# Kernel tuning notes

Hardware: AMD Instinct MI355X
Metric: run time of the kernel (lower is better)

## Reference

```python
import jax, jax.numpy as jnp
import numpy as np

B, Z, L = 256, 256, 8
C0, H0, W0 = 128, 8, 8
O = C0 * H0 * W0  # 8192


def _conv_transpose(x, w, b):
    """Torch ConvTranspose2d(k=4, s=2, p=1) equivalent.
    w: torch layout (in_ch, out_ch, kH, kW).
    Implemented as lhs-dilated conv with flipped, transposed kernel; pad = k-1-p = 2.
    """
    wt = jnp.flip(w, (2, 3)).transpose(1, 0, 2, 3)  # (out, in, kh, kw)
    y = jax.lax.conv_general_dilated(
        x, wt, window_strides=(1, 1), padding=[(2, 2), (2, 2)],
        lhs_dilation=(2, 2), dimension_numbers=('NCHW', 'OIHW', 'NCHW'))
    return y + b[None, :, None, None]


def setup_inputs() -> dict:
    key = jax.random.key(0)
    ks = jax.random.split(key, 6)
    return {
        'x': jax.random.normal(ks[0], (B, Z), jnp.float32),
        'gw': jax.random.normal(ks[1], (Z, L), jnp.float32) * (2.0 / (Z + L)) ** 0.5,  # xavier_normal
        'gb': jnp.zeros((L,), jnp.float32),
        'pw': jax.random.normal(ks[2], (O, Z, L), jnp.float32) * (1.0 / Z) ** 0.5,  # kaiming linear
        'pb': jnp.zeros((O, L), jnp.float32),
        'w1': jax.random.normal(ks[3], (C0, 64, 4, 4), jnp.float32) * 0.02,
        'b1': jnp.zeros((64,), jnp.float32),
        'w2': jax.random.normal(ks[4], (64, 32, 4, 4), jnp.float32) * 0.02,
        'b2': jnp.zeros((32,), jnp.float32),
        'w3': jax.random.normal(ks[5], (32, 3, 4, 4), jnp.float32) * 0.02,
        'b3': jnp.zeros((3,), jnp.float32),
    }


def reference(x, gw, gb, pw, pb, w1, b1, w2, b2, w3, b3):
    # --- ME mixture of linear experts (linear projection) ---
    g = jax.nn.softmax(x @ gw + gb, axis=1)               # (B, L)
    # Per-expert linear outputs, then gate-weighted sum. Mathematically equal to
    # torch's (pw @ gatings) per-sample weight followed by bmm with x, but avoids
    # the (B, O, Z) intermediate.
    expert_out = jnp.einsum('bi,oil->bol', x, pw)          # (B, O, L)
    out = jnp.einsum('bol,bl->bo', expert_out, g) + g @ pb.T  # (B, O)
    # --- conv-transpose decoder stack ---
    h = out.reshape(B, C0, H0, W0)
    h = jax.nn.relu(_conv_transpose(h, w1, b1))            # (B, 64, 16, 16)
    h = jax.nn.relu(_conv_transpose(h, w2, b2))            # (B, 32, 32, 32)
    h = _conv_transpose(h, w3, b3)                         # (B, 3, 64, 64)
    return h
```

## Files before the change

kernel.cpp:

```cpp
#include <hip/hip_runtime.h>

typedef __bf16 bf16;
typedef __bf16 bf16x8 __attribute__((ext_vector_type(8)));
typedef float f32x4 __attribute__((ext_vector_type(4)));

__device__ __forceinline__ f32x4 mfma16(bf16x8 a, bf16x8 b, f32x4 c) {
  return __builtin_amdgcn_mfma_f32_16x16x32_bf16(a, b, c, 0, 0, 0);
}

__device__ __forceinline__ void gload16(const void* g, void* l) {
  __builtin_amdgcn_global_load_lds(
      (const __attribute__((address_space(1))) void*)g,
      (__attribute__((address_space(3))) void*)(uint32_t)(size_t)l, 16, 0, 0);
}

__global__ __launch_bounds__(256) void gating_kernel(
    const float* __restrict__ x, const float* __restrict__ gw,
    const float* __restrict__ gb, bf16* __restrict__ xgb,
    float* __restrict__ gbuf) {
  const int b = blockIdx.x, tid = threadIdx.x;
  __shared__ float xs[256];
  __shared__ float gs[8];
  xs[tid] = x[b * 256 + tid];
  __syncthreads();
  if (tid < 8) {
    float acc = gb[tid];
    for (int i = 0; i < 256; ++i) acc += xs[i] * gw[i * 8 + tid];
    gs[tid] = acc;
  }
  __syncthreads();
  if (tid == 0) {
    float m = gs[0];
    for (int l = 1; l < 8; ++l) m = fmaxf(m, gs[l]);
    float s = 0.f, e[8];
    for (int l = 0; l < 8; ++l) { e[l] = expf(gs[l] - m); s += e[l]; }
    float inv = 1.f / s;
    for (int l = 0; l < 8; ++l) gs[l] = e[l] * inv;
  }
  __syncthreads();
  if (tid < 8) gbuf[b * 8 + tid] = gs[tid];
  bf16* dst = xgb + (size_t)b * 2048;
  for (int k = tid; k < 2048; k += 256)
    dst[k] = (bf16)(xs[k >> 3] * gs[k & 7]);
}

__global__ __launch_bounds__(256) void convert_pw_kernel(
    const float* __restrict__ pw, bf16* __restrict__ pwb) {
  const size_t base = (size_t)blockIdx.x * 2048 + threadIdx.x * 8;
  float4 v0 = *(const float4*)(pw + base);
  float4 v1 = *(const float4*)(pw + base + 4);
  bf16x8 r;
  r[0] = (bf16)v0.x; r[1] = (bf16)v0.y; r[2] = (bf16)v0.z; r[3] = (bf16)v0.w;
  r[4] = (bf16)v1.x; r[5] = (bf16)v1.y; r[6] = (bf16)v1.z; r[7] = (bf16)v1.w;
  *(bf16x8*)(pwb + base) = r;
}

template <int CIN, int COUT, int COUTP>
__global__ __launch_bounds__(256) void convert_w_kernel(
    const float* __restrict__ w, bf16* __restrict__ wp) {
  constexpr int K = 4 * CIN;
  constexpr int total = 4 * COUTP * K;
  int idx = blockIdx.x * 256 + threadIdx.x;
  if (idx >= total) return;
  int ic = idx & (CIN - 1);
  int t = (idx / CIN) & 3;
  int oc = (idx / K) % COUTP;
  int p = idx / (K * COUTP);
  bf16 v = (bf16)0.f;
  if (oc < COUT) {
    int py = p >> 1, px = p & 1, tyi = t >> 1, txi = t & 1;
    int ky = py == 0 ? (tyi ? 3 : 1) : (tyi ? 2 : 0);
    int kx = px == 0 ? (txi ? 3 : 1) : (txi ? 2 : 0);
    v = (bf16)w[((ic * COUT + oc) * 4 + ky) * 4 + kx];
  }
  wp[idx] = v;
}

template <int HP, int WP, int C>
__global__ __launch_bounds__(256) void border_zero_kernel(bf16* __restrict__ buf) {
  constexpr int NCELL = 2 * WP + 2 * (HP - 2);
  constexpr int C8 = C / 8;
  int idx = blockIdx.x * 256 + threadIdx.x;
  if (idx >= 256 * NCELL * C8) return;
  int c8 = idx % C8;
  int rem = idx / C8;
  int cell = rem % NCELL;
  int b = rem / NCELL;
  int y, x;
  if (cell < WP) { y = 0; x = cell; }
  else if (cell < 2 * WP) { y = HP - 1; x = cell - WP; }
  else { int r2 = cell - 2 * WP; y = 1 + (r2 >> 1); x = (r2 & 1) ? WP - 1 : 0; }
  bf16x8 z = {};
  *(bf16x8*)(buf + ((size_t)(b * HP + y) * WP + x) * C + c8 * 8) = z;
}

__global__ __launch_bounds__(256) void me_gemm_kernel(
    const bf16* __restrict__ pwb, const bf16* __restrict__ xgb,
    const float* __restrict__ pb, const float* __restrict__ gbuf,
    bf16* __restrict__ h0t) {
  __shared__ char sAB[32768];
  const int tid = threadIdx.x, wv = tid >> 6, l = tid & 63;
  const int lr = l & 15, lkg = l >> 4;
  const int wm = wv >> 1, wn = wv & 1;
  const int oM0 = blockIdx.x * 64, bN0 = blockIdx.y * 64;

  const int r1 = tid >> 3, cc1 = tid & 7;
  const int sb1 = (cc1 * 16) ^ ((r1 & 7) << 4);
  const int r2 = r1 + 32;
  const int sb2 = (cc1 * 16) ^ ((r2 & 7) << 4);
  const bf16* pA1 = pwb + (size_t)(oM0 + r1) * 2048 + (sb1 >> 1);
  const bf16* pA2 = pwb + (size_t)(oM0 + r2) * 2048 + (sb2 >> 1);
  const bf16* pB1 = xgb + (size_t)(bN0 + r1) * 2048 + (sb1 >> 1);
  const bf16* pB2 = xgb + (size_t)(bN0 + r2) * 2048 + (sb2 >> 1);
  char* lb0 = sAB + wv * 1024;

  gload16(pA1, lb0);
  gload16(pA2, lb0 + 4096);
  gload16(pB1, lb0 + 8192);
  gload16(pB2, lb0 + 12288);

  int raddrA[2][2], raddrB[2][2];
#pragma unroll
  for (int m = 0; m < 2; ++m) {
    int ra = wm * 32 + m * 16 + lr;
#pragma unroll
    for (int ks = 0; ks < 2; ++ks)
      raddrA[m][ks] = ra * 128 + ((ks * 64 + lkg * 16) ^ ((ra & 7) << 4));
  }
#pragma unroll
  for (int n = 0; n < 2; ++n) {
    int rb = wn * 32 + n * 16 + lr;
#pragma unroll
    for (int ks = 0; ks < 2; ++ks)
      raddrB[n][ks] = 8192 + rb * 128 + ((ks * 64 + lkg * 16) ^ ((rb & 7) << 4));
  }

  f32x4 acc[2][2] = {};
  __syncthreads();
#pragma unroll 2
  for (int kt = 0; kt < 32; ++kt) {
    const int cur = (kt & 1) * 16384;
    if (kt < 31) {
      char* lb = sAB + (((kt + 1) & 1) * 16384) + wv * 1024;
      const int ke = (kt + 1) * 64;
      gload16(pA1 + ke, lb);
      gload16(pA2 + ke, lb + 4096);
      gload16(pB1 + ke, lb + 8192);
      gload16(pB2 + ke, lb + 12288);
    }
    bf16x8 af[2][2], bfr[2][2];
#pragma unroll
    for (int ks = 0; ks < 2; ++ks) {
#pragma unroll
      for (int m = 0; m < 2; ++m)
        af[m][ks] = *(const bf16x8*)(sAB + cur + raddrA[m][ks]);
#pragma unroll
      for (int n = 0; n < 2; ++n)
        bfr[n][ks] = *(const bf16x8*)(sAB + cur + raddrB[n][ks]);
    }
#pragma unroll
    for (int ks = 0; ks < 2; ++ks)
#pragma unroll
      for (int m = 0; m < 2; ++m)
#pragma unroll
        for (int n = 0; n < 2; ++n)
          acc[m][n] = mfma16(af[m][ks], bfr[n][ks], acc[m][n]);
    __syncthreads();
  }

  float4 g0[2], g1[2];
#pragma unroll
  for (int n = 0; n < 2; ++n) {
    int b = bN0 + wn * 32 + n * 16 + lr;
    g0[n] = *(const float4*)(gbuf + b * 8);
    g1[n] = *(const float4*)(gbuf + b * 8 + 4);
  }
#pragma unroll
  for (int m = 0; m < 2; ++m)
#pragma unroll
    for (int r = 0; r < 4; ++r) {
      int o = oM0 + wm * 32 + m * 16 + lkg * 4 + r;
      float4 p0 = *(const float4*)(pb + o * 8);
      float4 p1 = *(const float4*)(pb + o * 8 + 4);
      int c = o >> 6, y = (o >> 3) & 7, xx = o & 7;
#pragma unroll
      for (int n = 0; n < 2; ++n) {
        int b = bN0 + wn * 32 + n * 16 + lr;
        float bias = g0[n].x * p0.x + g0[n].y * p0.y + g0[n].z * p0.z + g0[n].w * p0.w +
                     g1[n].x * p1.x + g1[n].y * p1.y + g1[n].z * p1.z + g1[n].w * p1.w;
        h0t[((size_t)(b * 10 + y + 1) * 10 + xx + 1) * 128 + c] = (bf16)(acc[m][n][r] + bias);
      }
    }
}

template <int CIN, int H, int YB, int COUTP, int WM, int NF, int SWM,
          bool WLDS, int INIT, int WIT, bool RELU, bool F32OUT, int SIN_SZ, int SW_SZ>
__global__ __launch_bounds__(256) void convt_kernel(
    const bf16* __restrict__ in, const bf16* __restrict__ wp,
    const float* __restrict__ bias, bf16* __restrict__ out,
    float* __restrict__ fout) {
  constexpr int W = H, WROW = W + 2, ROWB = CIN * 2, GRS = ROWB / 16;
  constexpr int LGR = (GRS == 16) ? 4 : (GRS == 8) ? 3 : 2;
  constexpr int LW = (W == 8) ? 3 : (W == 16) ? 4 : 5;
  constexpr int K = 4 * CIN;
  constexpr int CHUNKS = (YB + 2) * WROW * GRS;
  constexpr int WGR = K / 8;
  __shared__ char sIn[SIN_SZ];
  __shared__ char sW[SW_SZ];

  const int tid = threadIdx.x, wv = tid >> 6, l = tid & 63;
  const int nyb = H / YB;
  const int img = blockIdx.x / nyb, y0 = (blockIdx.x % nyb) * YB;
  const int p = blockIdx.y, py = p >> 1, px = p & 1;

#pragma unroll
  for (int it = 0; it < INIT; ++it) {
    int t = it * 256 + tid;
    int tc = t < CHUNKS ? t : CHUNKS - 1;
    int pix = tc >> LGR, cc = tc & (GRS - 1);
    int ly = pix / WROW, lx = pix % WROW;
    int sb = (cc * 16) ^ ((pix & SWM) << 4);
    gload16(in + ((size_t)((img * (H + 2) + y0 + ly) * (W + 2) + lx)) * CIN + (sb >> 1),
            sIn + it * 4096 + wv * 1024);
  }
  if constexpr (WLDS) {
#pragma unroll
    for (int it = 0; it < WIT; ++it) {
      int t = it * 256 + tid;
      int oc = t / WGR, cc = t % WGR;
      int sb = (cc * 16) ^ ((oc & 7) << 4);
      gload16(wp + (size_t)(p * COUTP + oc) * K + (sb >> 1), sW + it * 4096 + wv * 1024);
    }
  }
  __syncthreads();

  const int lr = l & 15, lkg = l >> 4;
  const int wm = wv & (WM - 1), wn = wv / WM;
  int pcen[2];
#pragma unroll
  for (int m = 0; m < 2; ++m) {
    int r = wm * 32 + m * 16 + lr;
    pcen[m] = ((r >> LW) + 1) * WROW + (r & (W - 1)) + 1;
  }

  f32x4 acc[2][NF] = {};
#pragma unroll 4
  for (int kk = 0; kk < K; kk += 32) {
    const int t4 = kk / CIN;
    const int tyi = t4 >> 1, txi = t4 & 1;
    const int dy = (py == 0) ? (tyi ? -1 : 0) : (tyi ? 0 : 1);
    const int dx = (px == 0) ? (txi ? -1 : 0) : (txi ? 0 : 1);
    const int icb = (kk % CIN) * 2 + lkg * 16;
    bf16x8 av[2], bv[NF];
#pragma unroll
    for (int m = 0; m < 2; ++m) {
      int pixd = pcen[m] + dy * WROW + dx;
      av[m] = *(const bf16x8*)(sIn + pixd * ROWB + (icb ^ ((pixd & SWM) << 4)));
    }
#pragma unroll
    for (int n = 0; n < NF; ++n) {
      int oc = (wn * NF + n) * 16 + lr;
      if constexpr (WLDS) {
        int kb = kk * 2 + lkg * 16;
        bv[n] = *(const bf16x8*)(sW + oc * (K * 2) + (kb ^ ((oc & 7) << 4)));
      } else {
        bv[n] = *(const bf16x8*)(wp + (size_t)(p * COUTP + oc) * K + kk + lkg * 8);
      }
    }
#pragma unroll
    for (int m = 0; m < 2; ++m)
#pragma unroll
      for (int n = 0; n < NF; ++n) acc[m][n] = mfma16(av[m], bv[n], acc[m][n]);
  }

#pragma unroll
  for (int m = 0; m < 2; ++m)
#pragma unroll
    for (int r4 = 0; r4 < 4; ++r4) {
      int r = wm * 32 + m * 16 + lkg * 4 + r4;
      int yy = r >> LW, xx = r & (W - 1);
      int oy = 2 * (y0 + yy) + py, ox = 2 * xx + px;
#pragma unroll
      for (int n = 0; n < NF; ++n) {
        int oc = (wn * NF + n) * 16 + lr;
        float v = acc[m][n][r4];
        if constexpr (F32OUT) {
          if (oc < 3) fout[((size_t)(img * 3 + oc) * (2 * H) + oy) * (2 * H) + ox] = v + bias[oc];
        } else {
          v += bias[oc];
          if constexpr (RELU) v = fmaxf(v, 0.f);
          out[((size_t)(img * (2 * H + 2) + oy + 1) * (2 * H + 2) + ox + 1) * COUTP + oc] = (bf16)v;
        }
      }
    }
}

extern "C" void kernel_launch(void* const* d_in, const int* in_sizes, int n_in,
                              void* d_out, int out_size, void* d_ws, size_t ws_size,
                              hipStream_t stream) {
  const float* x  = (const float*)d_in[0];
  const float* gw = (const float*)d_in[1];
  const float* gb = (const float*)d_in[2];
  const float* pw = (const float*)d_in[3];
  const float* pb = (const float*)d_in[4];
  const float* w1 = (const float*)d_in[5];
  const float* b1 = (const float*)d_in[6];
  const float* w2 = (const float*)d_in[7];
  const float* b2 = (const float*)d_in[8];
  const float* w3 = (const float*)d_in[9];
  const float* b3 = (const float*)d_in[10];
  float* outp = (float*)d_out;

  char* ws = (char*)d_ws;
  bf16*  xgb  = (bf16*)(ws + 0);
  float* gbuf = (float*)(ws + 1048576);
  bf16*  pwb  = (bf16*)(ws + 1056768);
  bf16*  h0t  = (bf16*)(ws + 34611200);
  bf16*  w1p  = (bf16*)(ws + 41164800);
  bf16*  h1   = (bf16*)(ws + 41426944);
  bf16*  w2p  = (bf16*)(ws + 52043776);
  bf16*  h2   = (bf16*)(ws + 52109312);
  bf16*  w3p  = (bf16*)(ws + 71049216);

  border_zero_kernel<10, 10, 128><<<576, 256, 0, stream>>>(h0t);
  border_zero_kernel<18, 18, 64><<<544, 256, 0, stream>>>(h1);
  border_zero_kernel<34, 34, 32><<<528, 256, 0, stream>>>(h2);

  gating_kernel<<<256, 256, 0, stream>>>(x, gw, gb, xgb, gbuf);
  convert_pw_kernel<<<8192, 256, 0, stream>>>(pw, pwb);
  convert_w_kernel<128, 64, 64><<<512, 256, 0, stream>>>(w1, w1p);
  convert_w_kernel<64, 32, 32><<<128, 256, 0, stream>>>(w2, w2p);
  convert_w_kernel<32, 3, 16><<<32, 256, 0, stream>>>(w3, w3p);

  me_gemm_kernel<<<dim3(128, 4), 256, 0, stream>>>(pwb, xgb, pb, gbuf, h0t);

  convt_kernel<128, 8, 8, 64, 2, 2, 7, false, 7, 0, true, false, 28672, 16>
      <<<dim3(256, 4), 256, 0, stream>>>(h0t, w1p, b1, h1, nullptr);
  convt_kernel<64, 16, 8, 32, 4, 2, 7, true, 6, 4, true, false, 24576, 16384>
      <<<dim3(512, 4), 256, 0, stream>>>(h1, w2p, b2, h2, nullptr);
  convt_kernel<32, 32, 4, 16, 4, 1, 3, true, 4, 1, false, true, 16384, 4096>
      <<<dim3(2048, 4), 256, 0, stream>>>(h2, w3p, b3, nullptr, outp);
}
```

Before: 122.0 us.

## Fuse pw fp32-to-bf16 conversion into ME GEMM and merge small prep kernels

```diff
diff --git a/kernel.cpp b/kernel.cpp
--- a/kernel.cpp
+++ b/kernel.cpp
@@ -2,6 +2,7 @@
 
 typedef __bf16 bf16;
 typedef __bf16 bf16x8 __attribute__((ext_vector_type(8)));
+typedef __bf16 bf16x4 __attribute__((ext_vector_type(4)));
 typedef float f32x4 __attribute__((ext_vector_type(4)));
 
 __device__ __forceinline__ f32x4 mfma16(bf16x8 a, bf16x8 b, f32x4 c) {
@@ -44,24 +45,10 @@
     dst[k] = (bf16)(xs[k >> 3] * gs[k & 7]);
 }
 
-__global__ __launch_bounds__(256) void convert_pw_kernel(
-    const float* __restrict__ pw, bf16* __restrict__ pwb) {
-  const size_t base = (size_t)blockIdx.x * 2048 + threadIdx.x * 8;
-  float4 v0 = *(const float4*)(pw + base);
-  float4 v1 = *(const float4*)(pw + base + 4);
-  bf16x8 r;
-  r[0] = (bf16)v0.x; r[1] = (bf16)v0.y; r[2] = (bf16)v0.z; r[3] = (bf16)v0.w;
-  r[4] = (bf16)v1.x; r[5] = (bf16)v1.y; r[6] = (bf16)v1.z; r[7] = (bf16)v1.w;
-  *(bf16x8*)(pwb + base) = r;
-}
-
 template <int CIN, int COUT, int COUTP>
-__global__ __launch_bounds__(256) void convert_w_kernel(
-    const float* __restrict__ w, bf16* __restrict__ wp) {
+__device__ __forceinline__ void cw_one(const float* __restrict__ w,
+                                       bf16* __restrict__ wp, int idx) {
   constexpr int K = 4 * CIN;
-  constexpr int total = 4 * COUTP * K;
-  int idx = blockIdx.x * 256 + threadIdx.x;
-  if (idx >= total) return;
   int ic = idx & (CIN - 1);
   int t = (idx / CIN) & 3;
   int oc = (idx / K) % COUTP;
@@ -76,12 +63,20 @@
   wp[idx] = v;
 }
 
+__global__ __launch_bounds__(256) void convert_w_all(
+    const float* __restrict__ w1, bf16* __restrict__ w1p,
+    const float* __restrict__ w2, bf16* __restrict__ w2p,
+    const float* __restrict__ w3, bf16* __restrict__ w3p) {
+  int idx = blockIdx.x * 256 + threadIdx.x;
+  if (idx < 131072) cw_one<128, 64, 64>(w1, w1p, idx);
+  else if (idx < 163840) cw_one<64, 32, 32>(w2, w2p, idx - 131072);
+  else if (idx < 172032) cw_one<32, 3, 16>(w3, w3p, idx - 163840);
+}
+
 template <int HP, int WP, int C>
-__global__ __launch_bounds__(256) void border_zero_kernel(bf16* __restrict__ buf) {
+__device__ __forceinline__ void bz_one(bf16* __restrict__ buf, int idx) {
   constexpr int NCELL = 2 * WP + 2 * (HP - 2);
   constexpr int C8 = C / 8;
-  int idx = blockIdx.x * 256 + threadIdx.x;
-  if (idx >= 256 * NCELL * C8) return;
   int c8 = idx % C8;
   int rem = idx / C8;
   int cell = rem % NCELL;
@@ -94,103 +89,104 @@
   *(bf16x8*)(buf + ((size_t)(b * HP + y) * WP + x) * C + c8 * 8) = z;
 }
 
-__global__ __launch_bounds__(256) void me_gemm_kernel(
-    const bf16* __restrict__ pwb, const bf16* __restrict__ xgb,
+__global__ __launch_bounds__(256) void border_zero_all(
+    bf16* __restrict__ h0t, bf16* __restrict__ h1, bf16* __restrict__ h2) {
+  int idx = blockIdx.x * 256 + threadIdx.x;
+  if (idx < 147456) bz_one<10, 10, 128>(h0t, idx);
+  else if (idx < 286720) bz_one<18, 18, 64>(h1, idx - 147456);
+  else if (idx < 421888) bz_one<34, 34, 32>(h2, idx - 286720);
+}
+
+__global__ __launch_bounds__(512) void me_gemm_kernel(
+    const float* __restrict__ pw, const bf16* __restrict__ xgb,
     const float* __restrict__ pb, const float* __restrict__ gbuf,
     bf16* __restrict__ h0t) {
-  __shared__ char sAB[32768];
+  __shared__ char sB[65536];
   const int tid = threadIdx.x, wv = tid >> 6, l = tid & 63;
   const int lr = l & 15, lkg = l >> 4;
-  const int wm = wv >> 1, wn = wv & 1;
-  const int oM0 = blockIdx.x * 64, bN0 = blockIdx.y * 64;
-
-  const int r1 = tid >> 3, cc1 = tid & 7;
-  const int sb1 = (cc1 * 16) ^ ((r1 & 7) << 4);
-  const int r2 = r1 + 32;
-  const int sb2 = (cc1 * 16) ^ ((r2 & 7) << 4);
-  const bf16* pA1 = pwb + (size_t)(oM0 + r1) * 2048 + (sb1 >> 1);
-  const bf16* pA2 = pwb + (size_t)(oM0 + r2) * 2048 + (sb2 >> 1);
-  const bf16* pB1 = xgb + (size_t)(bN0 + r1) * 2048 + (sb1 >> 1);
-  const bf16* pB2 = xgb + (size_t)(bN0 + r2) * 2048 + (sb2 >> 1);
-  char* lb0 = sAB + wv * 1024;
-
-  gload16(pA1, lb0);
-  gload16(pA2, lb0 + 4096);
-  gload16(pB1, lb0 + 8192);
-  gload16(pB2, lb0 + 12288);
-
-  int raddrA[2][2], raddrB[2][2];
-#pragma unroll
-  for (int m = 0; m < 2; ++m) {
-    int ra = wm * 32 + m * 16 + lr;
+  const int wm = wv & 1, wn = wv >> 1;
+  const int oM0 = blockIdx.x * 32;
+
+  const bf16* bsrc[4];
+  int bdst[4];
+#pragma unroll
+  for (int i = 0; i < 4; ++i) {
+    int ch = i * 512 + tid;
+    int r = ch >> 3, c = ch & 7;
+    int sb = (c * 16) ^ ((r & 7) << 4);
+    bsrc[i] = xgb + (size_t)r * 2048 + (sb >> 1);
+    bdst[i] = (i * 512 + wv * 64) * 16;
+  }
+  const float* pAf = pw + (size_t)(oM0 + wm * 16 + lr) * 2048 + lkg * 8;
+
+  int raddrB[4][2];
+#pragma unroll
+  for (int n = 0; n < 4; ++n) {
+    int rb = wn * 64 + n * 16 + lr;
 #pragma unroll
     for (int ks = 0; ks < 2; ++ks)
-      raddrA[m][ks] = ra * 128 + ((ks * 64 + lkg * 16) ^ ((ra & 7) << 4));
-  }
-#pragma unroll
-  for (int n = 0; n < 2; ++n) {
-    int rb = wn * 32 + n * 16 + lr;
+      raddrB[n][ks] = rb * 128 + ((ks * 64 + lkg * 16) ^ ((rb & 7) << 4));
+  }
+
+#pragma unroll
+  for (int i = 0; i < 4; ++i) gload16(bsrc[i], sB + bdst[i]);
+  float4 c0 = *(const float4*)(pAf);
+  float4 c1 = *(const float4*)(pAf + 4);
+  float4 c2 = *(const float4*)(pAf + 32);
+  float4 c3 = *(const float4*)(pAf + 36);
+
+  f32x4 acc[4] = {};
+  __syncthreads();
+  for (int kt = 0; kt < 32; ++kt) {
+    const int cur = (kt & 1) * 32768;
+    float4 n0, n1, n2, n3;
+    if (kt < 31) {
+      const int nb = ((kt + 1) & 1) * 32768;
+      const int ke = (kt + 1) * 64;
+#pragma unroll
+      for (int i = 0; i < 4; ++i) gload16(bsrc[i] + ke, sB + nb + bdst[i]);
+      n0 = *(const float4*)(pAf + ke);
+      n1 = *(const float4*)(pAf + ke + 4);
+      n2 = *(const float4*)(pAf + ke + 32);
+      n3 = *(const float4*)(pAf + ke + 36);
+    }
+    bf16x8 af[2];
+    af[0][0] = (bf16)c0.x; af[0][1] = (bf16)c0.y; af[0][2] = (bf16)c0.z; af[0][3] = (bf16)c0.w;
+    af[0][4] = (bf16)c1.x; af[0][5] = (bf16)c1.y; af[0][6] = (bf16)c1.z; af[0][7] = (bf16)c1.w;
+    af[1][0] = (bf16)c2.x; af[1][1] = (bf16)c2.y; af[1][2] = (bf16)c2.z; af[1][3] = (bf16)c2.w;
+    af[1][4] = (bf16)c3.x; af[1][5] = (bf16)c3.y; af[1][6] = (bf16)c3.z; af[1][7] = (bf16)c3.w;
 #pragma unroll
     for (int ks = 0; ks < 2; ++ks)
-      raddrB[n][ks] = 8192 + rb * 128 + ((ks * 64 + lkg * 16) ^ ((rb & 7) << 4));
-  }
-
-  f32x4 acc[2][2] = {};
-  __syncthreads();
-#pragma unroll 2
-  for (int kt = 0; kt < 32; ++kt) {
-    const int cur = (kt & 1) * 16384;
-    if (kt < 31) {
-      char* lb = sAB + (((kt + 1) & 1) * 16384) + wv * 1024;
-      const int ke = (kt + 1) * 64;
-      gload16(pA1 + ke, lb);
-      gload16(pA2 + ke, lb + 4096);
-      gload16(pB1 + ke, lb + 8192);
-      gload16(pB2 + ke, lb + 12288);
-    }
-    bf16x8 af[2][2], bfr[2][2];
-#pragma unroll
-    for (int ks = 0; ks < 2; ++ks) {
-#pragma unroll
-      for (int m = 0; m < 2; ++m)
-        af[m][ks] = *(const bf16x8*)(sAB + cur + raddrA[m][ks]);
-#pragma unroll
-      for (int n = 0; n < 2; ++n)
-        bfr[n][ks] = *(const bf16x8*)(sAB + cur + raddrB[n][ks]);
-    }
-#pragma unroll
-    for (int ks = 0; ks < 2; ++ks)
-#pragma unroll
-      for (int m = 0; m < 2; ++m)
-#pragma unroll
-        for (int n = 0; n < 2; ++n)
-          acc[m][n] = mfma16(af[m][ks], bfr[n][ks], acc[m][n]);
+#pragma unroll
+      for (int n = 0; n < 4; ++n) {
+        bf16x8 bv = *(const bf16x8*)(sB + cur + raddrB[n][ks]);
+        acc[n] = mfma16(af[ks], bv, acc[n]);
+      }
+    if (kt < 31) { c0 = n0; c1 = n1; c2 = n2; c3 = n3; }
     __syncthreads();
   }
 
-  float4 g0[2], g1[2];
-#pragma unroll
-  for (int n = 0; n < 2; ++n) {
-    int b = bN0 + wn * 32 + n * 16 + lr;
+  float4 g0[4], g1[4];
+#pragma unroll
+  for (int n = 0; n < 4; ++n) {
+    int b = wn * 64 + n * 16 + lr;
     g0[n] = *(const float4*)(gbuf + b * 8);
     g1[n] = *(const float4*)(gbuf + b * 8 + 4);
   }
 #pragma unroll
-  for (int m = 0; m < 2; ++m)
-#pragma unroll
-    for (int r = 0; r < 4; ++r) {
-      int o = oM0 + wm * 32 + m * 16 + lkg * 4 + r;
-      float4 p0 = *(const float4*)(pb + o * 8);
-      float4 p1 = *(const float4*)(pb + o * 8 + 4);
-      int c = o >> 6, y = (o >> 3) & 7, xx = o & 7;
-#pragma unroll
-      for (int n = 0; n < 2; ++n) {
-        int b = bN0 + wn * 32 + n * 16 + lr;
-        float bias = g0[n].x * p0.x + g0[n].y * p0.y + g0[n].z * p0.z + g0[n].w * p0.w +
-                     g1[n].x * p1.x + g1[n].y * p1.y + g1[n].z * p1.z + g1[n].w * p1.w;
-        h0t[((size_t)(b * 10 + y + 1) * 10 + xx + 1) * 128 + c] = (bf16)(acc[m][n][r] + bias);
-      }
-    }
+  for (int r = 0; r < 4; ++r) {
+    int o = oM0 + wm * 16 + lkg * 4 + r;
+    float4 p0 = *(const float4*)(pb + o * 8);
+    float4 p1 = *(const float4*)(pb + o * 8 + 4);
+    int cch = o >> 6, y = (o >> 3) & 7, xx = o & 7;
+#pragma unroll
+    for (int n = 0; n < 4; ++n) {
+      int b = wn * 64 + n * 16 + lr;
+      float bias = g0[n].x * p0.x + g0[n].y * p0.y + g0[n].z * p0.z + g0[n].w * p0.w +
+                   g1[n].x * p1.x + g1[n].y * p1.y + g1[n].z * p1.z + g1[n].w * p1.w;
+      h0t[((size_t)(b * 10 + y + 1) * 10 + xx + 1) * 128 + cch] = (bf16)(acc[n][r] + bias);
+    }
+  }
 }
 
 template <int CIN, int H, int YB, int COUTP, int WM, int NF, int SWM,
@@ -314,25 +310,18 @@
   char* ws = (char*)d_ws;
   bf16*  xgb  = (bf16*)(ws + 0);
   float* gbuf = (float*)(ws + 1048576);
-  bf16*  pwb  = (bf16*)(ws + 1056768);
-  bf16*  h0t  = (bf16*)(ws + 34611200);
-  bf16*  w1p  = (bf16*)(ws + 41164800);
-  bf16*  h1   = (bf16*)(ws + 41426944);
-  bf16*  w2p  = (bf16*)(ws + 52043776);
-  bf16*  h2   = (bf16*)(ws + 52109312);
-  bf16*  w3p  = (bf16*)(ws + 71049216);
-
-  border_zero_kernel<10, 10, 128><<<576, 256, 0, stream>>>(h0t);
-  border_zero_kernel<18, 18, 64><<<544, 256, 0, stream>>>(h1);
-  border_zero_kernel<34, 34, 32><<<528, 256, 0, stream>>>(h2);
-
+  bf16*  h0t  = (bf16*)(ws + 1056768);
+  bf16*  w1p  = (bf16*)(ws + 7610368);
+  bf16*  h1   = (bf16*)(ws + 7872512);
+  bf16*  w2p  = (bf16*)(ws + 18489344);
+  bf16*  h2   = (bf16*)(ws + 18554880);
+  bf16*  w3p  = (bf16*)(ws + 37494784);
+
+  border_zero_all<<<1648, 256, 0, stream>>>(h0t, h1, h2);
   gating_kernel<<<256, 256, 0, stream>>>(x, gw, gb, xgb, gbuf);
-  convert_pw_kernel<<<8192, 256, 0, stream>>>(pw, pwb);
-  convert_w_kernel<128, 64, 64><<<512, 256, 0, stream>>>(w1, w1p);
-  convert_w_kernel<64, 32, 32><<<128, 256, 0, stream>>>(w2, w2p);
-  convert_w_kernel<32, 3, 16><<<32, 256, 0, stream>>>(w3, w3p);
-
-  me_gemm_kernel<<<dim3(128, 4), 256, 0, stream>>>(pwb, xgb, pb, gbuf, h0t);
+  convert_w_all<<<672, 256, 0, stream>>>(w1, w1p, w2, w2p, w3, w3p);
+
+  me_gemm_kernel<<<256, 512, 0, stream>>>(pw, xgb, pb, gbuf, h0t);
 
   convt_kernel<128, 8, 8, 64, 2, 2, 7, false, 7, 0, true, false, 28672, 16>
       <<<dim3(256, 4), 256, 0, stream>>>(h0t, w1p, b1, h1, nullptr);
```

Result: slower. 128.3 us (+5.1%).
